# Optimization experiments

Hardware: AMD Instinct MI355X
Metric: run time of the kernel (lower is better)

## Reference

```python
import jax, jax.numpy as jnp
import numpy as np
from jax import lax


def setup_inputs() -> dict:
    key = jax.random.key(0)
    ks = jax.random.split(key, 20)
    B, T, Fin = 64, 360, 4
    C, H, W = 128, 32, 32          # encoder_hidden_dim, map size
    D, Hs, Ws = 128, 8, 8          # encoder_downsampled_dim, att feature map
    E, Hd, A, IF, O = 32, 128, 64, 128, 5
    IN = IF + C + E                # LSTMCell input size = 288
    s = 0.05
    # xy coords in [0, 0.31) so floor(v*100) is a valid index < 32
    prev_output_tokens = jax.random.uniform(ks[0], (B, T, Fin)) * 0.31 + 0.001
    feature = jax.random.normal(ks[1], (B, C, H, W))
    final_hidden = jax.random.normal(ks[2], (B, D, Hs, Ws))
    inp = dict(
        prev_output_tokens=prev_output_tokens,
        feature=feature,
        final_hidden=final_hidden,
        W_embed=jax.random.normal(ks[3], (Fin, E)) * s,
        b_embed=jnp.zeros((E,)),
        W_ih=jax.random.normal(ks[4], (IN, 4 * Hd)) * s,
        b_ih=jnp.zeros((4 * Hd,)),
        W_hh=jax.random.normal(ks[5], (Hd, 4 * Hd)) * s,
        b_hh=jnp.zeros((4 * Hd,)),
        W_h2att=jax.random.normal(ks[6], (Hd, A)) * s,
        b_h2att=jnp.zeros((A,)),
        W_alpha=jax.random.normal(ks[7], (A, 1)) * s,
        b_alpha=jnp.zeros((1,)),
        W_encproj=jax.random.normal(ks[8], (D, A)) * s,
        b_encproj=jnp.zeros((A,)),
        W_aap=jax.random.normal(ks[9], (Hd + D, IF)) * s,
        b_aap=jnp.zeros((IF,)),
        W_out=jax.random.normal(ks[10], (IF, O)) * s,
        b_out=jnp.zeros((O,)),
    )
    return inp


def reference(prev_output_tokens, feature, final_hidden,
              W_embed, b_embed, W_ih, b_ih, W_hh, b_hh,
              W_h2att, b_h2att, W_alpha, b_alpha,
              W_encproj, b_encproj, W_aap, b_aap, W_out, b_out):
    B, T, _ = prev_output_tokens.shape
    C, H = feature.shape[1], feature.shape[2]
    D = final_hidden.shape[1]
    Hd = W_hh.shape[0]
    IF = W_aap.shape[1]

    # embed_tokens (Linear)
    x_emb = prev_output_tokens @ W_embed + b_embed          # [B,T,E]

    # xy gather indices: floor(v*100), flat = y*H + x (torch uses size(-2))
    xy = (prev_output_tokens[..., :2] * 100).astype(jnp.int32)
    xy = jnp.where(xy == -1, 0, xy)
    idx = xy[..., 1] * H + xy[..., 0]                       # [B,T]
    feat_flat = feature.reshape(B, C, -1)                   # [B,C,H*W]

    # attention features and their projection (precomputed, as in torch)
    enc_feats = final_hidden.reshape(B, D, -1).transpose(0, 2, 1)   # [B,S,D]
    p_enc = enc_feats @ W_encproj + b_encproj                        # [B,S,A]

    def step(carry, xs):
        h, c, in_feed = carry
        xj, idxj = xs                                       # [B,E], [B]
        # gather encoder feature at the token's xy position
        in_seq = jnp.take_along_axis(feat_flat, idxj[:, None, None], axis=2)[..., 0]  # [B,C]
        inp = jnp.concatenate([xj, in_seq, in_feed], axis=-1)          # [B,288]
        # LSTMCell (torch gate order i,f,g,o)
        gates = inp @ W_ih + b_ih + h @ W_hh + b_hh
        i, f, g, o = jnp.split(gates, 4, axis=-1)
        c = jax.nn.sigmoid(f) * c + jax.nn.sigmoid(i) * jnp.tanh(g)
        h = jax.nn.sigmoid(o) * jnp.tanh(c)
        # additive attention
        att_h = h @ W_h2att + b_h2att                        # [B,A]
        dot = jnp.tanh(p_enc + att_h[:, None, :])            # [B,S,A]
        scores = (dot @ W_alpha)[..., 0] + b_alpha[0]        # [B,S]
        wgt = jax.nn.softmax(scores, axis=1)
        att_res = jnp.einsum('bs,bsd->bd', wgt, enc_feats)   # [B,D]
        out = jnp.concatenate([h, att_res], axis=-1) @ W_aap + b_aap  # [B,IF]
        return (h, c, out), out

    carry0 = (jnp.zeros((B, Hd), x_emb.dtype),
              jnp.zeros((B, Hd), x_emb.dtype),
              jnp.zeros((B, IF), x_emb.dtype))
    xs = (x_emb.transpose(1, 0, 2), idx.T)
    _, outs = lax.scan(step, carry0, xs)                     # [T,B,IF]
    x = outs.transpose(1, 0, 2)                              # [B,T,IF]
    return x @ W_out + b_out                                 # [B,T,5]
```

## Files before the change

### kernel.cpp

```cpp
#include <hip/hip_runtime.h>
#include <hip/hip_bf16.h>

#define BDIM 64
#define TDIM 360
#define BT (BDIM*TDIM)
#define CDIM 128
#define HWSZ 1024
#define SDIM 64
#define G4 512
#define KTOP 160

typedef __hip_bfloat16 bf16;
typedef __fp16 h2 __attribute__((ext_vector_type(2)));

static __device__ __forceinline__ unsigned int f2bu(float x) {
    bf16 b = __float2bfloat16(x);
    unsigned short u; __builtin_memcpy(&u, &b, 2); return (unsigned int)u;
}
static __device__ __forceinline__ float bl(unsigned int u) { return __uint_as_float(u << 16); }
static __device__ __forceinline__ float bh(unsigned int u) { return __uint_as_float(u & 0xffff0000u); }
static __device__ __forceinline__ h2 u2h(unsigned int u) {
    h2 r; __builtin_memcpy(&r, &u, 4); return r;
}
static __device__ __forceinline__ unsigned int packh(float a, float b) {
    h2 v = __builtin_amdgcn_cvt_pkrtz(a, b);
    unsigned int u; __builtin_memcpy(&u, &v, 4); return u;
}
static __device__ __forceinline__ float fdot2(unsigned int a, unsigned int b, float c) {
    return __builtin_amdgcn_fdot2(u2h(a), u2h(b), c, false);
}
static __device__ __forceinline__ float tanh_fast(float x) {
    float e = __expf(2.0f * x);
    return 1.0f - 2.0f / (e + 1.0f);
}
static __device__ __forceinline__ float sigm(float x) {
    return 1.0f / (1.0f + __expf(-x));
}

__device__ float        g_ArowsF[BT * KTOP];
__device__ float        g_pre2[BT * G4];
__device__ __align__(16) unsigned int g_wpk2[16 * 1024 * 4];
__device__ float        g_wrecA[128 * G4];
__device__ __align__(16) unsigned int g_encW2[BDIM * G4 * 32];
__device__ float        g_encWao[BDIM * 64 * 5];
__device__ float        g_penc[BDIM * SDIM * 64];
__device__ float        g_hw[BT * 192];
__device__ float        g_Wao[256 * 5];
__device__ float        g_bao[5];
__device__ float        g_bias[G4];
__device__ float        g_c0[G4];

__global__ void kA1(const float* __restrict__ tok, const float* __restrict__ feat,
                    const float* __restrict__ Wemb, const float* __restrict__ bemb) {
    int row  = blockIdx.x * 4 + (threadIdx.x >> 6);
    int lane = threadIdx.x & 63;
    const float* tp = tok + (size_t)row * 4;
    float t0 = tp[0], t1 = tp[1], t2 = tp[2], t3 = tp[3];
    int b = row / TDIM;
    int x = (int)(t0 * 100.0f);
    int y = (int)(t1 * 100.0f);
    x = min(max(x, 0), 31);
    y = min(max(y, 0), 31);
    int idx = y * 32 + x;
    float* out = g_ArowsF + (size_t)row * KTOP;
    if (lane < 32) {
        float e = t0 * Wemb[lane] + t1 * Wemb[32 + lane] +
                  t2 * Wemb[64 + lane] + t3 * Wemb[96 + lane] + bemb[lane];
        out[lane] = e;
    }
    const float* fb = feat + (size_t)b * CDIM * HWSZ + idx;
    out[32 + lane]      = fb[(size_t)lane * HWSZ];
    out[32 + 64 + lane] = fb[(size_t)(64 + lane) * HWSZ];
}

__global__ void kA2a(const float* __restrict__ Wih, const float* __restrict__ Whh,
                     const float* __restrict__ Waap) {
    __shared__ float sa0[128], sa1[128];
    int p = blockIdx.x, n = threadIdx.x;
    int r0 = 2 * p, r1 = 2 * p + 1;
    if (n < 128)            sa0[n]        = Waap[r0 * 128 + n];
    else if (n < 256)       sa1[n - 128]  = Waap[r1 * 128 + (n - 128)];
    __syncthreads();
    float acc0 = (r0 < 128) ? Whh[r0 * G4 + n] : 0.0f;
    float acc1 = (r1 < 128) ? Whh[r1 * G4 + n] : 0.0f;
    for (int j = 0; j < 128; ++j) {
        float wi = Wih[(160 + j) * G4 + n];
        acc0 += sa0[j] * wi;
        acc1 += sa1[j] * wi;
    }
    int kh = p >> 6, j = p & 63;
    int jblk = j >> 2, jj = j & 3;
    int u = kh * 512 + n;
    g_wpk2[((size_t)jblk * 1024 + u) * 4 + jj] = packh(acc0, acc1);
    if (p >= 64) {
        g_wrecA[(r0 - 128) * G4 + n] = acc0;
        g_wrecA[(r1 - 128) * G4 + n] = acc1;
    }
}

__global__ void kA2c(const float* __restrict__ bih, const float* __restrict__ bhh,
                     const float* __restrict__ Wih, const float* __restrict__ Waap,
                     const float* __restrict__ baap, const float* __restrict__ Wout,
                     const float* __restrict__ bout) {
    __shared__ float sb[128];
    int n = threadIdx.x;
    if (n < 128) sb[n] = baap[n];
    __syncthreads();
    g_bias[n] = bih[n] + bhh[n];
    float c0 = 0.0f;
    for (int j = 0; j < 128; ++j) c0 += sb[j] * Wih[(160 + j) * G4 + n];
    g_c0[n] = c0;
    if (n < 256) {
        for (int o = 0; o < 5; ++o) {
            float acc = 0.0f;
            for (int j = 0; j < 128; ++j) acc += Waap[n * 128 + j] * Wout[j * 5 + o];
            g_Wao[n * 5 + o] = acc;
        }
    }
    if (n == 0) {
        for (int o = 0; o < 5; ++o) {
            float acc = bout[o];
            for (int j = 0; j < 128; ++j) acc += sb[j] * Wout[j * 5 + o];
            g_bao[o] = acc;
        }
    }
}

__global__ void kA2d(const float* __restrict__ FH, const float* __restrict__ Wep,
                     const float* __restrict__ bep) {
    __shared__ float sfh[128 * 64];
    int b = blockIdx.x, tid = threadIdx.x;
    for (int i = tid; i < 128 * 64; i += 256) sfh[i] = FH[(size_t)b * 128 * 64 + i];
    __syncthreads();
    int a = tid & 63, sg = tid >> 6;
    float bias = bep[a];
    float acc[16];
#pragma unroll
    for (int i = 0; i < 16; ++i) acc[i] = bias;
    for (int d = 0; d < 128; ++d) {
        float wa = Wep[d * 64 + a];
#pragma unroll
        for (int i = 0; i < 16; ++i) acc[i] += sfh[d * 64 + sg * 16 + i] * wa;
    }
    for (int i = 0; i < 16; ++i)
        g_penc[((size_t)b * 64 + sg * 16 + i) * 64 + a] = acc[i];
}

__global__ void kA2e(const float* __restrict__ FH) {
    __shared__ float encL[64][129];
    int b = blockIdx.x, tid = threadIdx.x;
    for (int i = tid; i < 8192; i += 512) {
        int d = i >> 6, s = i & 63;
        encL[s][d] = FH[(size_t)b * 8192 + i];
    }
    __syncthreads();
    int n = tid;
#pragma unroll 1
    for (int sc = 0; sc < 8; ++sc) {
        float acc[8];
#pragma unroll
        for (int j = 0; j < 8; ++j) acc[j] = 0.f;
        for (int d = 0; d < 128; ++d) {
            float wv = g_wrecA[d * G4 + n];
#pragma unroll
            for (int j = 0; j < 8; ++j) acc[j] += encL[sc * 8 + j][d] * wv;
        }
#pragma unroll
        for (int j = 0; j < 4; ++j) {
            int s2 = sc * 4 + j;
            g_encW2[((size_t)b * G4 + n) * 32 + s2] = packh(acc[2 * j], acc[2 * j + 1]);
        }
    }
    if (tid < 64) {
        for (int o = 0; o < 5; ++o) {
            float acc = 0.f;
            for (int d = 0; d < 128; ++d)
                acc += encL[tid][d] * g_Wao[(128 + d) * 5 + o];
            g_encWao[((size_t)b * 64 + tid) * 5 + o] = acc;
        }
    }
}

__global__ void __attribute__((amdgpu_flat_work_group_size(512, 512),
                               amdgpu_waves_per_eu(2, 2)))
kB(const float* __restrict__ Wih) {
    int n = threadIdx.x;
    int m0 = blockIdx.x * 8;
    int pl = ((n & 127) << 2) | (n >> 7);
    float racc[8];
#pragma unroll
    for (int r = 0; r < 8; ++r) racc[r] = 0.0f;
#pragma unroll 1
    for (int pass = 0; pass < 2; ++pass) {
        float wcol[80];
#pragma unroll
        for (int j = 0; j < 80; ++j) wcol[j] = Wih[(pass * 80 + j) * G4 + n];
#pragma unroll
        for (int r = 0; r < 8; ++r) {
            const float4* rp = (const float4*)(g_ArowsF + (size_t)(m0 + r) * KTOP + pass * 80);
            float a0 = 0.f, a1 = 0.f, a2 = 0.f, a3 = 0.f;
#pragma unroll
            for (int q = 0; q < 20; ++q) {
                float4 v = rp[q];
                a0 += wcol[4 * q + 0] * v.x;
                a1 += wcol[4 * q + 1] * v.y;
                a2 += wcol[4 * q + 2] * v.z;
                a3 += wcol[4 * q + 3] * v.w;
            }
            racc[r] += (a0 + a1) + (a2 + a3);
        }
    }
#pragma unroll
    for (int r = 0; r < 8; ++r)
        g_pre2[(size_t)(m0 + r) * G4 + pl] = racc[r];
}

#define CONS1f(W, jb) { uint4 hp = hvals4[jb]; \
    acc0 = fdot2(W.x, hp.x, acc0); \
    acc1 = fdot2(W.y, hp.y, acc1); \
    acc0 = fdot2(W.z, hp.z, acc0); \
    acc1 = fdot2(W.w, hp.w, acc1); }
#define LDP(R, jb)  R = wp[(jb) * 1024];

#define SYNC() do { __builtin_amdgcn_sched_barrier(0); \
    asm volatile("s_waitcnt lgkmcnt(0)" ::: "memory"); \
    __builtin_amdgcn_s_barrier(); \
    __builtin_amdgcn_sched_barrier(0); } while (0)

__global__ void __launch_bounds__(512) kC(const float* __restrict__ Walpha,
                                          const float* __restrict__ balpha,
                                          const float* __restrict__ bh2a,
                                          const float* __restrict__ W2a) {
    __shared__ __align__(16) unsigned int s_h2[64];
    __shared__ __align__(16) float s_atth[64];
    __shared__ float s_scores[64];
    __shared__ __align__(16) unsigned int s_wgt2[32];
    __shared__ __align__(16) float s_walpha[64];
    __shared__ float s_bh2a[64];
    extern __shared__ __align__(16) char dsm[];
    unsigned int* s_encW  = (unsigned int*)dsm;
    float*        s_penc  = (float*)(dsm + 69632);
    unsigned int* s_w2aTp = (unsigned int*)(dsm + 69632 + 16640);

    int tid = threadIdx.x;
    int b = blockIdx.x;
    int lane = tid & 63;
    int qb = lane & ~3;
    int n = ((tid & 3) << 7) | (tid >> 2);
    int m = tid >> 2;

    const uint4* wp = ((const uint4*)g_wpk2) + n;
    uint4 P0,P1,P2,P3,P4,P5,P6,P7,P8,P9,P10,P11,P12,P13,P14,P15;
    LDP(P0,0)  LDP(P1,1)  LDP(P2,2)  LDP(P3,3)
    LDP(P4,4)  LDP(P5,5)  LDP(P6,6)  LDP(P7,7)
    LDP(P8,8)  LDP(P9,9)  LDP(P10,10) LDP(P11,11)
    LDP(P12,12) LDP(P13,13) LDP(P14,14) LDP(P15,15)

    float bias_r = g_bias[n];
    float bc_r   = bias_r + g_c0[n];
    float c_reg  = 0.0f;

    if (tid < 64) { s_h2[tid] = 0u; s_walpha[tid] = Walpha[tid]; s_bh2a[tid] = bh2a[tid]; }
    for (int i = tid; i < 16384; i += 512) {
        int row = i >> 5, s2 = i & 31;
        int loc = ((row & 127) << 2) | (row >> 7);
        s_encW[loc * 34 + s2] = g_encW2[(size_t)b * 16384 + i];
    }
    for (int i = tid; i < 4096; i += 512) {
        int s = i >> 6, a = i & 63;
        s_penc[s * 65 + a] = g_penc[((size_t)b * 64 + s) * 64 + a];
    }
    for (int i = tid; i < 4096; i += 512) {
        int a = i & 63, k2 = i >> 6;
        s_w2aTp[a * 68 + k2] = packh(W2a[(2 * k2) * 64 + a], W2a[(2 * k2 + 1) * 64 + a]);
    }
    float bal = balpha[0];

    const float* pre2p = g_pre2 + (size_t)b * TDIM * G4 + tid;
    float* hwp0 = g_hw + (size_t)b * TDIM * 192;

    for (int t = 0; t < TDIM; ++t) {
        SYNC();
        float pre2v = pre2p[(size_t)t * G4];
        float acc0 = 0.f, acc1 = 0.f;
        const uint4* hvals4 = (const uint4*)s_h2;
        CONS1f(P0,0)  CONS1f(P1,1)  CONS1f(P2,2)  CONS1f(P3,3)
        CONS1f(P4,4)  CONS1f(P5,5)  CONS1f(P6,6)  CONS1f(P7,7)
        CONS1f(P8,8)  CONS1f(P9,9)  CONS1f(P10,10) CONS1f(P11,11)
        CONS1f(P12,12) CONS1f(P13,13) CONS1f(P14,14) CONS1f(P15,15)
        float g = acc0 + acc1 + pre2v + (t ? bc_r : bias_r);
        if (t) {
            const uint2* er = (const uint2*)(s_encW + tid * 34);
            const uint2* wg = (const uint2*)s_wgt2;
            float w0 = 0.f, w1 = 0.f;
#pragma unroll
            for (int j = 0; j < 16; ++j) {
                uint2 ew = er[j], ww = wg[j];
                w0 = fdot2(ew.x, ww.x, w0);
                w1 = fdot2(ew.y, ww.y, w1);
            }
            g += w0 + w1;
        }
        {
            float gi = __shfl(g, qb + 0);
            float gf = __shfl(g, qb + 1);
            float gg = __shfl(g, qb + 2);
            float go = __shfl(g, qb + 3);
            float c = sigm(gf) * c_reg + sigm(gi) * tanh_fast(gg);
            c_reg = c;
            float h = sigm(go) * tanh_fast(c);
            if ((tid & 3) == 0) hwp0[(size_t)t * 192 + m] = h;
            float h_p = __shfl(h, lane ^ 4);
            if ((tid & 7) == 0) s_h2[tid >> 3] = packh(h, h_p);
        }
        SYNC();
        {
            int a = tid >> 3, sub = tid & 7;
            const uint4* hv = (const uint4*)s_h2;
            uint4 hA = hv[2 * sub], hB = hv[2 * sub + 1];
            const uint4* wr = (const uint4*)(s_w2aTp + a * 68 + 8 * sub);
            uint4 wA = wr[0], wB = wr[1];
            float a0 = 0.f, a1 = 0.f;
            a0 = fdot2(wA.x, hA.x, a0);  a1 = fdot2(wA.y, hA.y, a1);
            a0 = fdot2(wA.z, hA.z, a0);  a1 = fdot2(wA.w, hA.w, a1);
            a0 = fdot2(wB.x, hB.x, a0);  a1 = fdot2(wB.y, hB.y, a1);
            a0 = fdot2(wB.z, hB.z, a0);  a1 = fdot2(wB.w, hB.w, a1);
            float acc = a0 + a1;
            acc += __shfl_xor(acc, 1);
            acc += __shfl_xor(acc, 2);
            acc += __shfl_xor(acc, 4);
            if (sub == 0) s_atth[a] = acc + s_bh2a[a];
        }
        SYNC();
        {
            int ss = tid >> 3, sub = tid & 7;
            float acc = 0.f;
#pragma unroll
            for (int j = 0; j < 8; ++j) {
                int a = sub * 8 + j;
                float xv = s_penc[ss * 65 + a] + s_atth[a];
                acc += tanh_fast(xv) * s_walpha[a];
            }
            acc += __shfl_xor(acc, 1);
            acc += __shfl_xor(acc, 2);
            acc += __shfl_xor(acc, 4);
            if (sub == 0) s_scores[ss] = acc + bal;
        }
        SYNC();
        if (tid < 64) {
            float v = s_scores[tid];
            float mx = v;
#pragma unroll
            for (int off = 32; off > 0; off >>= 1) mx = fmaxf(mx, __shfl_xor(mx, off));
            float e = __expf(v - mx);
            float sum = e;
#pragma unroll
            for (int off = 32; off > 0; off >>= 1) sum += __shfl_xor(sum, off);
            float w = e / sum;
            hwp0[(size_t)t * 192 + 128 + tid] = w;
            float w_p = __shfl(w, lane ^ 1);
            if ((tid & 1) == 0) s_wgt2[tid >> 1] = packh(w, w_p);
        }
    }
}

__global__ void kD(float* __restrict__ out) {
    int r = blockIdx.x * 4 + (threadIdx.x >> 6);
    int lane = threadIdx.x & 63;
    int b = r / TDIM;
    float acc[5] = {0.f, 0.f, 0.f, 0.f, 0.f};
    if (lane < 48) {
        const float4* hv = (const float4*)(g_hw + (size_t)r * 192);
        float4 v = hv[lane];
        int k0 = lane * 4;
        if (lane < 32) {
#pragma unroll
            for (int o = 0; o < 5; ++o)
                acc[o] = v.x * g_Wao[(k0 + 0) * 5 + o] + v.y * g_Wao[(k0 + 1) * 5 + o] +
                         v.z * g_Wao[(k0 + 2) * 5 + o] + v.w * g_Wao[(k0 + 3) * 5 + o];
        } else {
            int s0 = k0 - 128;
            const float* ew = g_encWao + ((size_t)b * 64 + s0) * 5;
#pragma unroll
            for (int o = 0; o < 5; ++o)
                acc[o] = v.x * ew[o] + v.y * ew[5 + o] + v.z * ew[10 + o] + v.w * ew[15 + o];
        }
    }
#pragma unroll
    for (int off = 32; off > 0; off >>= 1) {
#pragma unroll
        for (int o = 0; o < 5; ++o) acc[o] += __shfl_xor(acc[o], off);
    }
    if (lane == 0) {
#pragma unroll
        for (int o = 0; o < 5; ++o) out[(size_t)r * 5 + o] = acc[o] + g_bao[o];
    }
}

extern "C" void kernel_launch(void* const* d_in, const int* in_sizes, int n_in,
                              void* d_out, int out_size, void* d_ws, size_t ws_size,
                              hipStream_t stream) {
    (void)in_sizes; (void)n_in; (void)d_ws; (void)ws_size; (void)out_size;
    const float* tok  = (const float*)d_in[0];
    const float* feat = (const float*)d_in[1];
    const float* FH   = (const float*)d_in[2];
    const float* Wemb = (const float*)d_in[3];
    const float* bemb = (const float*)d_in[4];
    const float* Wih  = (const float*)d_in[5];
    const float* bih  = (const float*)d_in[6];
    const float* Whh  = (const float*)d_in[7];
    const float* bhh  = (const float*)d_in[8];
    const float* W2a  = (const float*)d_in[9];
    const float* bh2a = (const float*)d_in[10];
    const float* Wal  = (const float*)d_in[11];
    const float* bal  = (const float*)d_in[12];
    const float* Wep  = (const float*)d_in[13];
    const float* bep  = (const float*)d_in[14];
    const float* Waap = (const float*)d_in[15];
    const float* baap = (const float*)d_in[16];
    const float* Wout = (const float*)d_in[17];
    const float* bout = (const float*)d_in[18];
    float* out = (float*)d_out;

    const int kc_dyn_lds = 69632 + 16640 + 17408;
    (void)hipFuncSetAttribute((const void*)kC,
                              hipFuncAttributeMaxDynamicSharedMemorySize,
                              kc_dyn_lds);

    kA1<<<dim3(BT / 4), dim3(256), 0, stream>>>(tok, feat, Wemb, bemb);
    kA2a<<<dim3(128), dim3(512), 0, stream>>>(Wih, Whh, Waap);
    kA2c<<<dim3(1), dim3(512), 0, stream>>>(bih, bhh, Wih, Waap, baap, Wout, bout);
    kA2d<<<dim3(64), dim3(256), 0, stream>>>(FH, Wep, bep);
    kA2e<<<dim3(BDIM), dim3(512), 0, stream>>>(FH);
    kB<<<dim3(BT / 8), dim3(512), 0, stream>>>(Wih);
    kC<<<dim3(64), dim3(512), kc_dyn_lds, stream>>>(Wal, bal, bh2a, W2a);
    kD<<<dim3(BT / 4), dim3(256), 0, stream>>>(out);
}
```

Before: 1.328 ms.

## Double-buffer hidden state and fuse attention projection with scoring to drop a barrier

The recurrent kernel now double-buffers the packed hidden state. Each wave recomputes the full 64-wide attention projection redundantly, one output per lane, and then computes scores for its own 8 positions with wave-wide shuffle reductions. This removes one block barrier per timestep and the shared att_h buffer, in exchange for redundant projection work in every wave and longer shuffle reduction chains. It also changes the launch attributes to request waves_per_eu of 2 and pads the transposed W2a layout differently.

```diff
diff --git a/kernel.cpp b/kernel.cpp
--- a/kernel.cpp
+++ b/kernel.cpp
@@ -17,8 +17,6 @@
     bf16 b = __float2bfloat16(x);
     unsigned short u; __builtin_memcpy(&u, &b, 2); return (unsigned int)u;
 }
-static __device__ __forceinline__ float bl(unsigned int u) { return __uint_as_float(u << 16); }
-static __device__ __forceinline__ float bh(unsigned int u) { return __uint_as_float(u & 0xffff0000u); }
 static __device__ __forceinline__ h2 u2h(unsigned int u) {
     h2 r; __builtin_memcpy(&r, &u, 4); return r;
 }
@@ -227,12 +225,13 @@
     __builtin_amdgcn_s_barrier(); \
     __builtin_amdgcn_sched_barrier(0); } while (0)
 
-__global__ void __launch_bounds__(512) kC(const float* __restrict__ Walpha,
-                                          const float* __restrict__ balpha,
-                                          const float* __restrict__ bh2a,
-                                          const float* __restrict__ W2a) {
-    __shared__ __align__(16) unsigned int s_h2[64];
-    __shared__ __align__(16) float s_atth[64];
+__global__ void __attribute__((amdgpu_flat_work_group_size(512, 512),
+                               amdgpu_waves_per_eu(2, 2)))
+kC(const float* __restrict__ Walpha,
+   const float* __restrict__ balpha,
+   const float* __restrict__ bh2a,
+   const float* __restrict__ W2a) {
+    __shared__ __align__(16) unsigned int s_h2[2][64];
     __shared__ float s_scores[64];
     __shared__ __align__(16) unsigned int s_wgt2[32];
     __shared__ __align__(16) float s_walpha[64];
@@ -248,6 +247,7 @@
     int qb = lane & ~3;
     int n = ((tid & 3) << 7) | (tid >> 2);
     int m = tid >> 2;
+    int w = tid >> 6;
 
     const uint4* wp = ((const uint4*)g_wpk2) + n;
     uint4 P0,P1,P2,P3,P4,P5,P6,P7,P8,P9,P10,P11,P12,P13,P14,P15;
@@ -260,7 +260,7 @@
     float bc_r   = bias_r + g_c0[n];
     float c_reg  = 0.0f;
 
-    if (tid < 64) { s_h2[tid] = 0u; s_walpha[tid] = Walpha[tid]; s_bh2a[tid] = bh2a[tid]; }
+    if (tid < 64) { s_h2[0][tid] = 0u; s_walpha[tid] = Walpha[tid]; s_bh2a[tid] = bh2a[tid]; }
     for (int i = tid; i < 16384; i += 512) {
         int row = i >> 5, s2 = i & 31;
         int loc = ((row & 127) << 2) | (row >> 7);
@@ -272,7 +272,7 @@
     }
     for (int i = tid; i < 4096; i += 512) {
         int a = i & 63, k2 = i >> 6;
-        s_w2aTp[a * 68 + k2] = packh(W2a[(2 * k2) * 64 + a], W2a[(2 * k2 + 1) * 64 + a]);
+        s_w2aTp[a * 66 + k2] = packh(W2a[(2 * k2) * 64 + a], W2a[(2 * k2 + 1) * 64 + a]);
     }
     float bal = balpha[0];
 
@@ -280,10 +280,11 @@
     float* hwp0 = g_hw + (size_t)b * TDIM * 192;
 
     for (int t = 0; t < TDIM; ++t) {
+        int cur = t & 1, nxt = cur ^ 1;
         SYNC();
         float pre2v = pre2p[(size_t)t * G4];
         float acc0 = 0.f, acc1 = 0.f;
-        const uint4* hvals4 = (const uint4*)s_h2;
+        const uint4* hvals4 = (const uint4*)(&s_h2[cur][0]);
         CONS1f(P0,0)  CONS1f(P1,1)  CONS1f(P2,2)  CONS1f(P3,3)
         CONS1f(P4,4)  CONS1f(P5,5)  CONS1f(P6,6)  CONS1f(P7,7)
         CONS1f(P8,8)  CONS1f(P9,9)  CONS1f(P10,10) CONS1f(P11,11)
@@ -311,40 +312,33 @@
             float h = sigm(go) * tanh_fast(c);
             if ((tid & 3) == 0) hwp0[(size_t)t * 192 + m] = h;
             float h_p = __shfl(h, lane ^ 4);
-            if ((tid & 7) == 0) s_h2[tid >> 3] = packh(h, h_p);
+            if ((tid & 7) == 0) s_h2[nxt][tid >> 3] = packh(h, h_p);
         }
         SYNC();
         {
-            int a = tid >> 3, sub = tid & 7;
-            const uint4* hv = (const uint4*)s_h2;
-            uint4 hA = hv[2 * sub], hB = hv[2 * sub + 1];
-            const uint4* wr = (const uint4*)(s_w2aTp + a * 68 + 8 * sub);
-            uint4 wA = wr[0], wB = wr[1];
+            int a = lane;
+            const uint2* hv2 = (const uint2*)(&s_h2[nxt][0]);
+            const uint2* wr  = (const uint2*)(s_w2aTp + a * 66);
             float a0 = 0.f, a1 = 0.f;
-            a0 = fdot2(wA.x, hA.x, a0);  a1 = fdot2(wA.y, hA.y, a1);
-            a0 = fdot2(wA.z, hA.z, a0);  a1 = fdot2(wA.w, hA.w, a1);
-            a0 = fdot2(wB.x, hB.x, a0);  a1 = fdot2(wB.y, hB.y, a1);
-            a0 = fdot2(wB.z, hB.z, a0);  a1 = fdot2(wB.w, hB.w, a1);
-            float acc = a0 + a1;
-            acc += __shfl_xor(acc, 1);
-            acc += __shfl_xor(acc, 2);
-            acc += __shfl_xor(acc, 4);
-            if (sub == 0) s_atth[a] = acc + s_bh2a[a];
-        }
-        SYNC();
-        {
-            int ss = tid >> 3, sub = tid & 7;
-            float acc = 0.f;
+#pragma unroll
+            for (int j = 0; j < 16; ++j) {
+                uint2 wv = wr[j], hh = hv2[j];
+                a0 = fdot2(wv.x, hh.x, a0);
+                a1 = fdot2(wv.y, hh.y, a1);
+            }
+            float atv = a0 + a1 + s_bh2a[a];
 #pragma unroll
             for (int j = 0; j < 8; ++j) {
-                int a = sub * 8 + j;
-                float xv = s_penc[ss * 65 + a] + s_atth[a];
-                acc += tanh_fast(xv) * s_walpha[a];
+                int ss = w * 8 + j;
+                float val = tanh_fast(s_penc[ss * 65 + a] + atv) * s_walpha[a];
+                val += __shfl_xor(val, 1);
+                val += __shfl_xor(val, 2);
+                val += __shfl_xor(val, 4);
+                val += __shfl_xor(val, 8);
+                val += __shfl_xor(val, 16);
+                val += __shfl_xor(val, 32);
+                if (lane == 0) s_scores[ss] = val + bal;
             }
-            acc += __shfl_xor(acc, 1);
-            acc += __shfl_xor(acc, 2);
-            acc += __shfl_xor(acc, 4);
-            if (sub == 0) s_scores[ss] = acc + bal;
         }
         SYNC();
         if (tid < 64) {
@@ -356,10 +350,10 @@
             float sum = e;
 #pragma unroll
             for (int off = 32; off > 0; off >>= 1) sum += __shfl_xor(sum, off);
-            float w = e / sum;
-            hwp0[(size_t)t * 192 + 128 + tid] = w;
-            float w_p = __shfl(w, lane ^ 1);
-            if ((tid & 1) == 0) s_wgt2[tid >> 1] = packh(w, w_p);
+            float wv = e / sum;
+            hwp0[(size_t)t * 192 + 128 + tid] = wv;
+            float w_p = __shfl(wv, lane ^ 1);
+            if ((tid & 1) == 0) s_wgt2[tid >> 1] = packh(wv, w_p);
         }
     }
 }
@@ -422,7 +416,7 @@
     const float* bout = (const float*)d_in[18];
     float* out = (float*)d_out;
 
-    const int kc_dyn_lds = 69632 + 16640 + 17408;
+    const int kc_dyn_lds = 69632 + 16640 + 16896;
     (void)hipFuncSetAttribute((const void*)kC,
                               hipFuncAttributeMaxDynamicSharedMemorySize,
                               kc_dyn_lds);
```

Measured after the change: 1.902 ms. +43.2%, slower.
